# Kernel optimization log

Hardware: AMD Instinct MI355X
Metric: run time of the kernel (lower is better)

Reference implementation:

```python
import jax, jax.numpy as jnp
import numpy as np

N_NODES = 100000
MAX_DEG = 16
D_IN = 256
D_OUT = 256


def setup_inputs() -> dict:
    key = jax.random.key(0)
    k1, k2, k3, k4, k5 = jax.random.split(key, 5)
    x = jax.random.normal(k1, (N_NODES, D_IN), dtype=jnp.float32)
    # padded edge list: -1 marks padding; first column always valid so degree >= 1
    col0 = jax.random.randint(k2, (N_NODES, 1), 0, N_NODES)
    rest = jax.random.randint(k3, (N_NODES, MAX_DEG - 1), -1, N_NODES)
    edge_index = jnp.concatenate([col0, rest], axis=1).astype(jnp.int64)
    # torch Linear(2*D_IN, D_OUT): weight [D_OUT, 2*D_IN], bias [D_OUT]
    W = jax.random.normal(k4, (D_OUT, 2 * D_IN), dtype=jnp.float32) * 0.05
    b = jax.random.normal(k5, (D_OUT,), dtype=jnp.float32) * 0.05
    return {"x": x, "edge_index": edge_index, "W": W, "b": b}


def reference(x, edge_index, W, b):
    # pad with a zero row so index -1 (padding) gathers zeros, matching torch
    padded = jnp.concatenate([x, jnp.zeros((1, x.shape[1]), dtype=x.dtype)], axis=0)
    neigh = padded[edge_index]  # [N, MAX_DEG, D_IN]
    degree = jnp.sum(edge_index >= 0, axis=-1, keepdims=True).astype(x.dtype)  # [N, 1]
    neigh_agg = jnp.sum(neigh, axis=1) / degree  # mean aggregation, [N, D_IN]
    h = jnp.concatenate([x, neigh_agg], axis=1)  # [N, 2*D_IN]
    return h @ W.T + b
```

## Files before the change

### kernel.cpp

```cpp
#include <hip/hip_runtime.h>
#include <stdint.h>


#define MAX_DEG 16
#define D_IN 256
#define D_OUT 256
#define N_NODES_C 100000

typedef __attribute__((ext_vector_type(8))) short bf16x8;
typedef __attribute__((ext_vector_type(4))) float f32x4;

__device__ __forceinline__ uint32_t f2bf(float f) {
    union { float f; uint32_t u; } v; v.f = f;
    uint32_t u = v.u;
    return (u + 0x7FFFu + ((u >> 16) & 1u)) >> 16;
}
__device__ __forceinline__ uint32_t pack2(float lo, float hi) {
    return f2bf(lo) | (f2bf(hi) << 16);
}

__global__ __launch_bounds__(256) void cast_w2_kernel(
    const float* __restrict__ W, ushort* __restrict__ Wb2, ushort* __restrict__ y2)
{
    const int b = blockIdx.x;
    const int tid = threadIdx.x;
    if (b < 128) {
        const int idx = (b * 256 + tid) * 4;
        const int c = idx >> 8;
        const int k = idx & 255;
        const float4 v = *(const float4*)(W + (size_t)(c & 255) * 512 + (c >> 8) * 256 + k);
        ushort4 p = { (ushort)f2bf(v.x), (ushort)f2bf(v.y),
                      (ushort)f2bf(v.z), (ushort)f2bf(v.w) };
        *(ushort4*)(Wb2 + (size_t)c * 256 + k) = p;
    } else {
        if (tid < 32) {
            uint4 z = {0u, 0u, 0u, 0u};
            *(uint4*)(y2 + (size_t)N_NODES_C * 256 + tid * 8) = z;
        }
    }
}

#define LDS_A_STRIDE 264

__global__ __launch_bounds__(512, 4) void gemm_xw_kernel(
    const float* __restrict__ x, const ushort* __restrict__ Wb2,
    const float* __restrict__ bias, ushort* __restrict__ y2,
    float* __restrict__ out)
{
    __shared__ ushort sA[32 * LDS_A_STRIDE];

    const int tid = threadIdx.x;
    const int node0 = blockIdx.x * 32;

    {
        const int m = tid >> 4;
        const int l = tid & 15;
        const float4* xr = (const float4*)(x + (size_t)(node0 + m) * D_IN) + l * 4;
        float4 v0 = xr[0], v1 = xr[1], v2 = xr[2], v3 = xr[3];
        uint4 p0 = { pack2(v0.x, v0.y), pack2(v0.z, v0.w),
                     pack2(v1.x, v1.y), pack2(v1.z, v1.w) };
        uint4 p1 = { pack2(v2.x, v2.y), pack2(v2.z, v2.w),
                     pack2(v3.x, v3.y), pack2(v3.z, v3.w) };
        uint4* dst = (uint4*)(sA + (size_t)m * LDS_A_STRIDE + l * 16);
        dst[0] = p0; dst[1] = p1;
    }
    __syncthreads();

    const int w = tid >> 6;
    const int lane = tid & 63;
    const int quad = lane >> 4;
    const int r16  = lane & 15;

    f32x4 acc[2][4];
    #pragma unroll
    for (int mt = 0; mt < 2; ++mt)
        #pragma unroll
        for (int j = 0; j < 4; ++j)
            acc[mt][j] = (f32x4){0.f, 0.f, 0.f, 0.f};

    const ushort* a0p = sA + (size_t)r16 * LDS_A_STRIDE + quad * 8;
    const ushort* a1p = a0p + 16 * LDS_A_STRIDE;
    #pragma unroll
    for (int ks = 0; ks < D_IN / 32; ++ks) {
        bf16x8 a0 = *(const bf16x8*)(a0p + ks * 32);
        bf16x8 a1 = *(const bf16x8*)(a1p + ks * 32);
        #pragma unroll
        for (int j = 0; j < 4; ++j) {
            const int c = w * 64 + j * 16 + r16;
            bf16x8 b = *(const bf16x8*)(Wb2 + (size_t)c * 256 + ks * 32 + quad * 8);
            acc[0][j] = __builtin_amdgcn_mfma_f32_16x16x32_bf16(a0, b, acc[0][j], 0, 0, 0);
            acc[1][j] = __builtin_amdgcn_mfma_f32_16x16x32_bf16(a1, b, acc[1][j], 0, 0, 0);
        }
    }

    if (w < 4) {
        #pragma unroll
        for (int j = 0; j < 4; ++j) {
            const int c = w * 64 + j * 16 + r16;
            const float bv = bias[c];
            #pragma unroll
            for (int mt = 0; mt < 2; ++mt)
                #pragma unroll
                for (int r = 0; r < 4; ++r) {
                    const int row = node0 + mt * 16 + quad * 4 + r;
                    out[(size_t)row * D_OUT + c] = acc[mt][j][r] + bv;
                }
        }
    } else {
        #pragma unroll
        for (int j = 0; j < 4; ++j) {
            const int c2 = (w - 4) * 64 + j * 16 + r16;
            #pragma unroll
            for (int mt = 0; mt < 2; ++mt)
                #pragma unroll
                for (int r = 0; r < 4; ++r) {
                    const int row = node0 + mt * 16 + quad * 4 + r;
                    y2[(size_t)row * 256 + c2] = (ushort)f2bf(acc[mt][j][r]);
                }
        }
    }
}

__global__ __launch_bounds__(256, 6) void gather_add_kernel(
    const ushort* __restrict__ y2, const int* __restrict__ edge,
    float* __restrict__ out)
{
    const int i = blockIdx.x * 4 + (threadIdx.x >> 6);
    const int lane = threadIdx.x & 63;

    const int e = edge[(size_t)i * MAX_DEG + (lane & 15)];
    const unsigned long long vm = __ballot(e >= 0);
    const int deg = (int)__popcll(vm & 0xFFFFull);
    const float inv = 1.0f / (float)deg;

    const uint32_t off_me = (uint32_t)(e < 0 ? N_NODES_C : e) * 512u;
    const char* yb = (const char*)y2;
    const uint32_t coff = (uint32_t)((lane & 31) * 16);

    uint32_t off[8];
    #pragma unroll
    for (int k = 0; k < 8; ++k)
        off[k] = (uint32_t)__shfl((int)off_me, 2 * k + (lane >> 5), 64);

    uint4 g[8];
    #pragma unroll
    for (int k = 0; k < 8; ++k)
        g[k] = *(const uint4*)(yb + (size_t)(off[k] + coff));

    float a[8];
    #pragma unroll
    for (int q = 0; q < 8; ++q) a[q] = 0.f;
    #pragma unroll
    for (int k = 0; k < 8; ++k) {
        uint32_t u[4] = { g[k].x, g[k].y, g[k].z, g[k].w };
        #pragma unroll
        for (int q = 0; q < 4; ++q) {
            union { uint32_t ui; float f; } lo, hi;
            lo.ui = u[q] << 16;
            hi.ui = u[q] & 0xFFFF0000u;
            a[2*q]   += lo.f;
            a[2*q+1] += hi.f;
        }
    }
    #pragma unroll
    for (int q = 0; q < 8; ++q) a[q] += __shfl_xor(a[q], 32, 64);

    const int cw = (lane & 31) * 8 + (lane >> 5) * 4;
    const int q0 = (lane >> 5) * 4;
    float4 yv = *(const float4*)(out + (size_t)i * D_OUT + cw);
    float4 r;
    r.x = yv.x + inv * a[q0 + 0];
    r.y = yv.y + inv * a[q0 + 1];
    r.z = yv.z + inv * a[q0 + 2];
    r.w = yv.w + inv * a[q0 + 3];
    *(float4*)(out + (size_t)i * D_OUT + cw) = r;
}

#define D_K 512
#define LDS_STRIDE 520

__global__ __launch_bounds__(256) void cast_w_kernel(const float* __restrict__ W,
                                                     ushort* __restrict__ Wb) {
    int i = (blockIdx.x * 256 + threadIdx.x) * 4;
    float4 v = *(const float4*)(W + i);
    ushort4 p = { (ushort)f2bf(v.x), (ushort)f2bf(v.y),
                  (ushort)f2bf(v.z), (ushort)f2bf(v.w) };
    *(ushort4*)(Wb + i) = p;
}

__global__ __launch_bounds__(256) void sage_fp32_kernel(
    const float* __restrict__ x, const int* __restrict__ edge,
    const ushort* __restrict__ Wb, const float* __restrict__ bias,
    float* __restrict__ out)
{
    __shared__ ushort sH[32 * LDS_STRIDE];
    const int tid = threadIdx.x;
    const int node0 = blockIdx.x * 32;
    {
        const int m = tid >> 3, l = tid & 7;
        const int node = node0 + m;
        const float4* xrow = (const float4*)(x + (size_t)node * D_IN);
        ushort* dst = sH + m * LDS_STRIDE + l * 32;
        #pragma unroll
        for (int q = 0; q < 8; ++q) {
            float4 v = xrow[l * 8 + q];
            ushort4 p = { (ushort)f2bf(v.x), (ushort)f2bf(v.y),
                          (ushort)f2bf(v.z), (ushort)f2bf(v.w) };
            *(ushort4*)(dst + q * 4) = p;
        }
        float4 agg[8];
        #pragma unroll
        for (int q = 0; q < 8; ++q) agg[q] = make_float4(0.f,0.f,0.f,0.f);
        int deg = 0;
        for (int d = 0; d < MAX_DEG; ++d) {
            int nb = edge[(size_t)node * MAX_DEG + d];
            if (nb >= 0) {
                ++deg;
                const float4* nr = (const float4*)(x + (size_t)nb * D_IN);
                #pragma unroll
                for (int q = 0; q < 8; ++q) {
                    float4 t = nr[l * 8 + q];
                    agg[q].x += t.x; agg[q].y += t.y;
                    agg[q].z += t.z; agg[q].w += t.w;
                }
            }
        }
        const float inv = 1.0f / (float)deg;
        ushort* dst2 = sH + m * LDS_STRIDE + D_IN + l * 32;
        #pragma unroll
        for (int q = 0; q < 8; ++q) {
            ushort4 p = { (ushort)f2bf(agg[q].x*inv), (ushort)f2bf(agg[q].y*inv),
                          (ushort)f2bf(agg[q].z*inv), (ushort)f2bf(agg[q].w*inv) };
            *(ushort4*)(dst2 + q * 4) = p;
        }
    }
    __syncthreads();
    {
        const int wave = tid >> 6, lane = tid & 63;
        const int quad = lane >> 4, r16 = lane & 15;
        const int mt = wave & 1, nh = wave >> 1;
        f32x4 acc[8];
        #pragma unroll
        for (int j = 0; j < 8; ++j) {
            float bv = bias[(nh * 8 + j) * 16 + r16];
            acc[j] = (f32x4){bv, bv, bv, bv};
        }
        const ushort* arow = sH + (mt * 16 + r16) * LDS_STRIDE + quad * 8;
        #pragma unroll
        for (int ks = 0; ks < D_K / 32; ++ks) {
            bf16x8 a = *(const bf16x8*)(arow + ks * 32);
            #pragma unroll
            for (int j = 0; j < 8; ++j) {
                const int o = (nh * 8 + j) * 16 + r16;
                bf16x8 b = *(const bf16x8*)(Wb + (size_t)o * D_K + ks * 32 + quad * 8);
                acc[j] = __builtin_amdgcn_mfma_f32_16x16x32_bf16(a, b, acc[j], 0, 0, 0);
            }
        }
        #pragma unroll
        for (int j = 0; j < 8; ++j) {
            const int o = (nh * 8 + j) * 16 + r16;
            #pragma unroll
            for (int r = 0; r < 4; ++r) {
                const int row = node0 + mt * 16 + quad * 4 + r;
                out[(size_t)row * D_OUT + o] = acc[j][r];
            }
        }
    }
}

extern "C" void kernel_launch(void* const* d_in, const int* in_sizes, int n_in,
                              void* d_out, int out_size, void* d_ws, size_t ws_size,
                              hipStream_t stream) {
    const float* x    = (const float*)d_in[0];
    const int*   edge = (const int*)d_in[1];
    const float* W    = (const float*)d_in[2];
    const float* bias = (const float*)d_in[3];
    float* out = (float*)d_out;

    const size_t y2_bytes = (size_t)(N_NODES_C + 1) * 256 * 2;
    const size_t wb_bytes = (size_t)512 * 256 * 2;
    const int n = in_sizes[0] / D_IN;

    if (ws_size >= y2_bytes + wb_bytes) {
        ushort* y2  = (ushort*)d_ws;
        ushort* Wb2 = (ushort*)((char*)d_ws + y2_bytes);
        cast_w2_kernel<<<129, 256, 0, stream>>>(W, Wb2, y2);
        gemm_xw_kernel<<<n / 32, 512, 0, stream>>>(x, Wb2, bias, y2, out);
        gather_add_kernel<<<n / 4, 256, 0, stream>>>(y2, edge, out);
    } else {
        ushort* Wb = (ushort*)d_ws;
        cast_w_kernel<<<(D_OUT * D_K) / 1024, 256, 0, stream>>>(W, Wb);
        sage_fp32_kernel<<<n / 32, 256, 0, stream>>>(x, edge, Wb, bias, out);
    }
}
```

Baseline: 407.3 us.

## Double GEMM row tile to 64 and pre-swizzle bf16 weights into MFMA fragment order

The GEMM block now covers 64 nodes instead of 32, so each weight fragment loaded from global memory feeds four MFMAs instead of two, halving total weight traffic per output. The weight cast kernel writes W in a fragment-major layout so each wave reads contiguous 16-byte lanes with simple offsets. A tail guard handles N not divisible by 64. This costs more accumulator registers (64 floats per lane) and doubles LDS per block, which may reduce occupancy.

```diff
diff --git a/kernel.cpp b/kernel.cpp
--- a/kernel.cpp
+++ b/kernel.cpp
@@ -6,6 +6,8 @@
 #define D_IN 256
 #define D_OUT 256
 #define N_NODES_C 100000
+#define BM 64
+#define LDS_A_STRIDE 264
 
 typedef __attribute__((ext_vector_type(8))) short bf16x8;
 typedef __attribute__((ext_vector_type(4))) float f32x4;
@@ -19,50 +21,55 @@
     return f2bf(lo) | (f2bf(hi) << 16);
 }
 
-__global__ __launch_bounds__(256) void cast_w2_kernel(
-    const float* __restrict__ W, ushort* __restrict__ Wb2, ushort* __restrict__ y2)
+__global__ __launch_bounds__(256) void cast_w2f_kernel(
+    const float* __restrict__ W, ushort* __restrict__ Wb2f, ushort* __restrict__ y2)
 {
-    const int b = blockIdx.x;
-    const int tid = threadIdx.x;
-    if (b < 128) {
-        const int idx = (b * 256 + tid) * 4;
-        const int c = idx >> 8;
-        const int k = idx & 255;
-        const float4 v = *(const float4*)(W + (size_t)(c & 255) * 512 + (c >> 8) * 256 + k);
-        ushort4 p = { (ushort)f2bf(v.x), (ushort)f2bf(v.y),
-                      (ushort)f2bf(v.z), (ushort)f2bf(v.w) };
-        *(ushort4*)(Wb2 + (size_t)c * 256 + k) = p;
+    if (blockIdx.x < 64) {
+        const int t = blockIdx.x * 256 + threadIdx.x;
+        const int cg   = t >> 9;
+        const int ks   = (t >> 6) & 7;
+        const int lane = t & 63;
+        const int quad = lane >> 4, r16 = lane & 15;
+        const int c = cg * 16 + r16;
+        const int k = ks * 32 + quad * 8;
+        const float* src = W + (size_t)(c & 255) * 512 + (c >> 8) * 256 + k;
+        float4 v0 = ((const float4*)src)[0];
+        float4 v1 = ((const float4*)src)[1];
+        uint4 p = { pack2(v0.x, v0.y), pack2(v0.z, v0.w),
+                    pack2(v1.x, v1.y), pack2(v1.z, v1.w) };
+        *(uint4*)(Wb2f + (size_t)t * 8) = p;
     } else {
-        if (tid < 32) {
+        if (threadIdx.x < 32) {
             uint4 z = {0u, 0u, 0u, 0u};
-            *(uint4*)(y2 + (size_t)N_NODES_C * 256 + tid * 8) = z;
-        }
-    }
-}
-
-#define LDS_A_STRIDE 264
+            *(uint4*)(y2 + (size_t)N_NODES_C * 256 + threadIdx.x * 8) = z;
+        }
+    }
+}
 
 __global__ __launch_bounds__(512, 4) void gemm_xw_kernel(
-    const float* __restrict__ x, const ushort* __restrict__ Wb2,
+    const float* __restrict__ x, const ushort* __restrict__ Wb2f,
     const float* __restrict__ bias, ushort* __restrict__ y2,
     float* __restrict__ out)
 {
-    __shared__ ushort sA[32 * LDS_A_STRIDE];
+    __shared__ ushort sA[BM * LDS_A_STRIDE];
 
     const int tid = threadIdx.x;
-    const int node0 = blockIdx.x * 32;
+    const int node0 = blockIdx.x * BM;
 
     {
-        const int m = tid >> 4;
-        const int l = tid & 15;
-        const float4* xr = (const float4*)(x + (size_t)(node0 + m) * D_IN) + l * 4;
-        float4 v0 = xr[0], v1 = xr[1], v2 = xr[2], v3 = xr[3];
-        uint4 p0 = { pack2(v0.x, v0.y), pack2(v0.z, v0.w),
-                     pack2(v1.x, v1.y), pack2(v1.z, v1.w) };
-        uint4 p1 = { pack2(v2.x, v2.y), pack2(v2.z, v2.w),
-                     pack2(v3.x, v3.y), pack2(v3.z, v3.w) };
-        uint4* dst = (uint4*)(sA + (size_t)m * LDS_A_STRIDE + l * 16);
-        dst[0] = p0; dst[1] = p1;
+        #pragma unroll
+        for (int it = 0; it < 4; ++it) {
+            const int idx = it * 512 + tid;
+            const int row = idx >> 5;
+            const int c8  = idx & 31;
+            const int rg  = node0 + row;
+            const float* src = x + (size_t)(rg < N_NODES_C ? rg : N_NODES_C - 1) * D_IN + c8 * 8;
+            float4 v0 = ((const float4*)src)[0];
+            float4 v1 = ((const float4*)src)[1];
+            uint4 p = { pack2(v0.x, v0.y), pack2(v0.z, v0.w),
+                        pack2(v1.x, v1.y), pack2(v1.z, v1.w) };
+            *(uint4*)(sA + (size_t)row * LDS_A_STRIDE + c8 * 8) = p;
+        }
     }
     __syncthreads();
 
@@ -71,25 +78,29 @@
     const int quad = lane >> 4;
     const int r16  = lane & 15;
 
-    f32x4 acc[2][4];
-    #pragma unroll
-    for (int mt = 0; mt < 2; ++mt)
+    f32x4 acc[4][4];
+    #pragma unroll
+    for (int s = 0; s < 4; ++s)
         #pragma unroll
         for (int j = 0; j < 4; ++j)
-            acc[mt][j] = (f32x4){0.f, 0.f, 0.f, 0.f};
-
-    const ushort* a0p = sA + (size_t)r16 * LDS_A_STRIDE + quad * 8;
-    const ushort* a1p = a0p + 16 * LDS_A_STRIDE;
+            acc[s][j] = (f32x4){0.f, 0.f, 0.f, 0.f};
+
+    const ushort* ap = sA + (size_t)r16 * LDS_A_STRIDE + quad * 8;
+    const ushort* bp = Wb2f + ((size_t)(w * 4) * 8 + 0) * 64 * 8 + lane * 8;
+
     #pragma unroll
     for (int ks = 0; ks < D_IN / 32; ++ks) {
-        bf16x8 a0 = *(const bf16x8*)(a0p + ks * 32);
-        bf16x8 a1 = *(const bf16x8*)(a1p + ks * 32);
+        bf16x8 a0 = *(const bf16x8*)(ap + 0  * 16 * LDS_A_STRIDE + ks * 32);
+        bf16x8 a1 = *(const bf16x8*)(ap + 1  * 16 * LDS_A_STRIDE + ks * 32);
+        bf16x8 a2 = *(const bf16x8*)(ap + 2  * 16 * LDS_A_STRIDE + ks * 32);
+        bf16x8 a3 = *(const bf16x8*)(ap + 3  * 16 * LDS_A_STRIDE + ks * 32);
         #pragma unroll
         for (int j = 0; j < 4; ++j) {
-            const int c = w * 64 + j * 16 + r16;
-            bf16x8 b = *(const bf16x8*)(Wb2 + (size_t)c * 256 + ks * 32 + quad * 8);
+            bf16x8 b = *(const bf16x8*)(bp + ((size_t)j * 8 + ks) * 64 * 8);
             acc[0][j] = __builtin_amdgcn_mfma_f32_16x16x32_bf16(a0, b, acc[0][j], 0, 0, 0);
             acc[1][j] = __builtin_amdgcn_mfma_f32_16x16x32_bf16(a1, b, acc[1][j], 0, 0, 0);
+            acc[2][j] = __builtin_amdgcn_mfma_f32_16x16x32_bf16(a2, b, acc[2][j], 0, 0, 0);
+            acc[3][j] = __builtin_amdgcn_mfma_f32_16x16x32_bf16(a3, b, acc[3][j], 0, 0, 0);
         }
     }
 
@@ -99,11 +110,12 @@
             const int c = w * 64 + j * 16 + r16;
             const float bv = bias[c];
             #pragma unroll
-            for (int mt = 0; mt < 2; ++mt)
+            for (int s = 0; s < 4; ++s)
                 #pragma unroll
                 for (int r = 0; r < 4; ++r) {
-                    const int row = node0 + mt * 16 + quad * 4 + r;
-                    out[(size_t)row * D_OUT + c] = acc[mt][j][r] + bv;
+                    const int row = node0 + s * 16 + quad * 4 + r;
+                    if (row < N_NODES_C)
+                        out[(size_t)row * D_OUT + c] = acc[s][j][r] + bv;
                 }
         }
     } else {
@@ -111,11 +123,12 @@
         for (int j = 0; j < 4; ++j) {
             const int c2 = (w - 4) * 64 + j * 16 + r16;
             #pragma unroll
-            for (int mt = 0; mt < 2; ++mt)
+            for (int s = 0; s < 4; ++s)
                 #pragma unroll
                 for (int r = 0; r < 4; ++r) {
-                    const int row = node0 + mt * 16 + quad * 4 + r;
-                    y2[(size_t)row * 256 + c2] = (ushort)f2bf(acc[mt][j][r]);
+                    const int row = node0 + s * 16 + quad * 4 + r;
+                    if (row < N_NODES_C)
+                        y2[(size_t)row * 256 + c2] = (ushort)f2bf(acc[s][j][r]);
                 }
         }
     }
@@ -282,10 +295,10 @@
     const int n = in_sizes[0] / D_IN;
 
     if (ws_size >= y2_bytes + wb_bytes) {
-        ushort* y2  = (ushort*)d_ws;
-        ushort* Wb2 = (ushort*)((char*)d_ws + y2_bytes);
-        cast_w2_kernel<<<129, 256, 0, stream>>>(W, Wb2, y2);
-        gemm_xw_kernel<<<n / 32, 512, 0, stream>>>(x, Wb2, bias, y2, out);
+        ushort* y2   = (ushort*)d_ws;
+        ushort* Wb2f = (ushort*)((char*)d_ws + y2_bytes);
+        cast_w2f_kernel<<<65, 256, 0, stream>>>(W, Wb2f, y2);
+        gemm_xw_kernel<<<(n + BM - 1) / BM, 512, 0, stream>>>(x, Wb2f, bias, y2, out);
         gather_add_kernel<<<n / 4, 256, 0, stream>>>(y2, edge, out);
     } else {
         ushort* Wb = (ushort*)d_ws;
```

Result: faster. 380.2 us (-6.7%).
